# Kernel optimization log

Measured on AMD Instinct MI355X. Metric: run time of the kernel, lower is better.

## Reference

```python
import jax, jax.numpy as jnp
import numpy as np

N_CHUNK = 8
CHUNK = 128
HID = 1024

def cumsoftmax(x):
    return jnp.cumsum(jax.nn.softmax(x, axis=-1), axis=-1)

def setup_inputs() -> dict:
    key = jax.random.key(0)
    ks = jax.random.split(key, 4)
    L, B, D = 512, 64, HID
    G = 4 * HID + 2 * N_CHUNK  # 4112
    x = jax.random.normal(ks[0], (L, B, D), dtype=jnp.float32)
    h0 = jnp.zeros((2, B, HID), jnp.float32)
    c0 = jnp.zeros((2, B, N_CHUNK, CHUNK), jnp.float32)
    Wih = jax.random.normal(ks[1], (2, D, G), dtype=jnp.float32) * 0.02
    bih = jnp.zeros((2, G), jnp.float32)
    Whh = jax.random.normal(ks[2], (2, HID, G), dtype=jnp.float32) * 0.02
    bhh = jnp.zeros((2, G), jnp.float32)
    return {"x": x, "h0": h0, "c0": c0, "Wih": Wih, "bih": bih, "Whh": Whh, "bhh": bhh}

def _run_layer(prev, h, c, wih, b_ih, whh, b_hh):
    nc, cs = N_CHUNK, CHUNK
    # precompute input transform for all timesteps: [L,B,G]
    t_in = jnp.einsum('lbd,dg->lbg', prev, wih) + b_ih

    def step(carry, ti):
        hx, cx = carry
        gates = ti + hx @ whh + b_hh            # [B, G]
        cingate = 1.0 - cumsoftmax(gates[:, :nc])
        cforget = cumsoftmax(gates[:, nc:2 * nc])
        rest = gates[:, 2 * nc:].reshape(-1, 4 * nc, cs)
        outg, cell, ing, fg = jnp.split(rest, 4, axis=1)  # each [B,nc,cs]
        d_forget = 1.0 - cforget.sum(-1) / nc   # [B]? no: sum over nc -> [B]
        d_in = cingate.sum(-1) / nc
        cing = cingate[:, :, None]
        cfg = cforget[:, :, None]
        ing = jax.nn.sigmoid(ing)
        fg = jax.nn.sigmoid(fg)
        cell = jnp.tanh(cell)
        outg = jax.nn.sigmoid(outg)
        overlap = cfg * cing
        fg = fg * overlap + (cfg - overlap)
        ing = ing * overlap + (cing - overlap)
        cy = fg * cx + ing * cell
        hy = (outg * jnp.tanh(cy)).reshape(-1, HID)
        return (hy, cy), (hy, d_forget, d_in)

    (hT, cT), (hs, dfs, dins) = jax.lax.scan(step, (h, c), t_in)
    return hs, hT, cT, dfs, dins

def reference(x, h0, c0, Wih, bih, Whh, bhh):
    prev = x
    hTs, cTs, outs, dfs_l, dins_l = [], [], [], [], []
    for l in range(Wih.shape[0]):
        hs, hT, cT, dfs, dins = _run_layer(prev, h0[l], c0[l], Wih[l], bih[l], Whh[l], bhh[l])
        prev = hs  # dropout=0.0 / eval mode: LockedDropout is identity
        outs.append(hs)
        hTs.append(hT)
        cTs.append(cT)
        dfs_l.append(dfs)
        dins_l.append(dins)
    output = prev                                   # [L,B,H]
    return (output,
            jnp.stack(hTs), jnp.stack(cTs),         # final states per layer
            jnp.stack(outs),                        # raw_outputs == outputs (no dropout)
            jnp.stack(dfs_l), jnp.stack(dins_l))    # distances [n_layers,L,B]
```

## Files before the change

kernel.cpp:

```cpp
#include <hip/hip_runtime.h>
#include <math.h>

#define LSEQ 512
#define BATCH 64
#define HID 1024
#define NCH 8
#define GSZ 4112
#define NB2 128

typedef __bf16 bf16x8 __attribute__((ext_vector_type(8)));
typedef float f32x4 __attribute__((ext_vector_type(4)));
typedef unsigned u32x4 __attribute__((ext_vector_type(4)));
typedef unsigned u32x2 __attribute__((ext_vector_type(2)));

__device__ __forceinline__ ushort f2b(float f) {
  union { float f; unsigned u; } v; v.f = f;
  unsigned u = v.u;
  unsigned r = (u + 0x7FFFu + ((u >> 16) & 1u)) >> 16;
  return (ushort)r;
}
__device__ __forceinline__ float b2f(ushort h) {
  union { unsigned u; float f; } v; v.u = (unsigned)h << 16; return v.f;
}
__device__ __forceinline__ float sigmoidf(float x) { return 1.f / (1.f + expf(-x)); }

__global__ __launch_bounds__(256) void k_transpose_cast(
    const float* __restrict__ W, ushort* __restrict__ WT, int K, int N) {
  __shared__ float tile[32][33];
  int n0 = blockIdx.x * 32, k0 = blockIdx.y * 32;
  int tx = threadIdx.x & 31, ty = threadIdx.x >> 5;
  #pragma unroll
  for (int i = ty; i < 32; i += 8) {
    int n = n0 + tx;
    tile[i][tx] = (n < N) ? W[(size_t)(k0 + i) * N + n] : 0.f;
  }
  __syncthreads();
  #pragma unroll
  for (int i = ty; i < 32; i += 8) {
    int n = n0 + i;
    if (n < N) WT[(size_t)n * K + k0 + tx] = f2b(tile[tx][i]);
  }
}

__global__ void k_cast4(const float4* __restrict__ in, ushort* __restrict__ out, int count4) {
  int stride = gridDim.x * blockDim.x;
  for (int i = blockIdx.x * blockDim.x + threadIdx.x; i < count4; i += stride) {
    float4 v = in[i];
    ushort4 o;
    o.x = f2b(v.x); o.y = f2b(v.y); o.z = f2b(v.z); o.w = f2b(v.w);
    *reinterpret_cast<ushort4*>(out + (size_t)i * 4) = o;
  }
}

__global__ void k_init2(const float* __restrict__ h0, const float* __restrict__ c0,
                        ushort* __restrict__ h1b1, ushort* __restrict__ h2b1,
                        float* __restrict__ c1, float* __restrict__ c2,
                        unsigned* __restrict__ barmem) {
  int i = blockIdx.x * blockDim.x + threadIdx.x;
  const int n = BATCH * HID;
  if (i < n) { h1b1[i] = f2b(h0[i]); c1[i] = c0[i]; }
  else if (i < 2 * n) {
    int j = i - n;
    h2b1[j] = f2b(h0[n + j]); c2[j] = c0[n + j];
  }
  if (i < NB2 * 16) barmem[i] = 0u;
}

__global__ __launch_bounds__(256) void k_gemm_t(
    const ushort* __restrict__ A, const ushort* __restrict__ BT,
    const float* __restrict__ bias, ushort* __restrict__ Ct, int K, int N) {
  int col0 = blockIdx.x * 64;
  int t = blockIdx.y;
  int lane = threadIdx.x & 63;
  int w = threadIdx.x >> 6;
  int l15 = lane & 15;
  int koff = (lane >> 4) * 8;
  const ushort* Ap = A + (size_t)(t * 64 + w * 16 + l15) * K + koff;
  const ushort* Bp[4];
  int cols[4];
  #pragma unroll
  for (int cg = 0; cg < 4; ++cg) {
    int c_ = col0 + cg * 16 + l15;
    cols[cg] = c_;
    int cc = c_ < N ? c_ : N - 1;
    Bp[cg] = BT + (size_t)cc * K + koff;
  }
  f32x4 acc[4] = {};
  #pragma unroll 4
  for (int kk = 0; kk < K; kk += 32) {
    bf16x8 a = *reinterpret_cast<const bf16x8*>(Ap + kk);
    #pragma unroll
    for (int cg = 0; cg < 4; ++cg) {
      bf16x8 b = *reinterpret_cast<const bf16x8*>(Bp[cg] + kk);
      acc[cg] = __builtin_amdgcn_mfma_f32_16x16x32_bf16(a, b, acc[cg], 0, 0, 0);
    }
  }
  int crow = w * 16 + (lane >> 4) * 4;
  #pragma unroll
  for (int cg = 0; cg < 4; ++cg) {
    int c_ = cols[cg];
    if (c_ >= N) continue;
    float bv = bias[c_];
    ushort4 o;
    o.x = f2b(acc[cg][0] + bv); o.y = f2b(acc[cg][1] + bv);
    o.z = f2b(acc[cg][2] + bv); o.w = f2b(acc[cg][3] + bv);
    *reinterpret_cast<ushort4*>(&Ct[((size_t)t * GSZ + c_) * 64 + crow]) = o;
  }
}

__global__ __launch_bounds__(1024, 2) void k_scan2(
    const ushort* __restrict__ WhhT0, const ushort* __restrict__ WhhT1,
    const ushort* __restrict__ WihT1,
    const float* __restrict__ bhh0, const float* __restrict__ bhh1,
    const float* __restrict__ bih1,
    const ushort* __restrict__ tin,
    ushort* __restrict__ h1b0, ushort* __restrict__ h1b1,
    ushort* __restrict__ h2b0, ushort* __restrict__ h2b1,
    float* __restrict__ c1, float* __restrict__ c2,
    float* __restrict__ outs0, float* __restrict__ outs1,
    float* __restrict__ outdup,
    float* __restrict__ dfs0, float* __restrict__ dins0,
    float* __restrict__ dfs1, float* __restrict__ dins1,
    float* __restrict__ hT0, float* __restrict__ cT0,
    float* __restrict__ hT1, float* __restrict__ cT1,
    unsigned* __restrict__ barmem, int nsteps, int t0, int barbase) {
  __shared__ unsigned hlds[32768];
  __shared__ __align__(16) float gbuf[80][68];

  const int tid = threadIdx.x;
  const int blk = blockIdx.x;
  const bool isL2 = blk >= 64;
  const int lblk = isL2 ? (blk - 64) : blk;
  const int j0 = lblk * 16;
  const int lane = tid & 63;
  const int w = tid >> 6;
  const int l15 = lane & 15;
  const int lg = lane >> 4;
  const int koff = lg * 8;

  const int ct = (w < 5) ? w : 0;
  const int gcol = (ct == 0) ? l15 : (16 + (ct - 1) * 1024 + j0 + l15);
  const int grow = (ct == 0) ? l15 : (16 + (ct - 1) * 16 + l15);
  const ushort* bpA = (isL2 ? WhhT1 : WhhT0) + (size_t)gcol * HID + koff;
  const ushort* bpB = WihT1 + (size_t)gcol * HID + koff;
  const float bv = isL2 ? (bhh1[gcol] + bih1[gcol]) : bhh0[gcol];
  const int cr = lg * 4;
  const unsigned ab = (unsigned)l15 * 2048u + (unsigned)(lg * 16);
  const unsigned swz = (unsigned)(l15 & 7) << 4;

  const int cb = tid >> 4;
  const int jl = tid & 15;
  const int jglob = j0 + jl;
  const int rch = jglob >> 7;
  float creg = (isL2 ? c2 : c1)[cb * HID + jglob];

  float* out_my  = isL2 ? outs1 : outs0;
  float* dfs_my  = isL2 ? dfs1  : dfs0;
  float* dins_my = isL2 ? dins1 : dins0;

  float def_hy = 0.f, def_df = 0.f, def_di = 0.f;
  size_t def_oidx = 0;
  int def_didx = 0;
  bool have_def = false;

#define LOAD8(hbase) do { \
    const u32x4* hs_ = (const u32x4*)(hbase); \
    asm volatile("global_load_dwordx4 %0, %1, off sc0 sc1" : "=v"(z0) : "v"(hs_ + tid)        : "memory"); \
    asm volatile("global_load_dwordx4 %0, %1, off sc0 sc1" : "=v"(z1) : "v"(hs_ + tid + 1024) : "memory"); \
    asm volatile("global_load_dwordx4 %0, %1, off sc0 sc1" : "=v"(z2) : "v"(hs_ + tid + 2048) : "memory"); \
    asm volatile("global_load_dwordx4 %0, %1, off sc0 sc1" : "=v"(z3) : "v"(hs_ + tid + 3072) : "memory"); \
    asm volatile("global_load_dwordx4 %0, %1, off sc0 sc1" : "=v"(z4) : "v"(hs_ + tid + 4096) : "memory"); \
    asm volatile("global_load_dwordx4 %0, %1, off sc0 sc1" : "=v"(z5) : "v"(hs_ + tid + 5120) : "memory"); \
    asm volatile("global_load_dwordx4 %0, %1, off sc0 sc1" : "=v"(z6) : "v"(hs_ + tid + 6144) : "memory"); \
    asm volatile("global_load_dwordx4 %0, %1, off sc0 sc1" : "=v"(z7) : "v"(hs_ + tid + 7168) : "memory"); \
  } while (0)

#define WRITE8() do { \
    unsigned b_; \
    b_ = (unsigned)tid * 16u;          *(u32x4*)((char*)hlds + (b_ ^ (((b_ >> 11) & 7u) << 4))) = z0; \
    b_ = (unsigned)(tid + 1024) * 16u; *(u32x4*)((char*)hlds + (b_ ^ (((b_ >> 11) & 7u) << 4))) = z1; \
    b_ = (unsigned)(tid + 2048) * 16u; *(u32x4*)((char*)hlds + (b_ ^ (((b_ >> 11) & 7u) << 4))) = z2; \
    b_ = (unsigned)(tid + 3072) * 16u; *(u32x4*)((char*)hlds + (b_ ^ (((b_ >> 11) & 7u) << 4))) = z3; \
    b_ = (unsigned)(tid + 4096) * 16u; *(u32x4*)((char*)hlds + (b_ ^ (((b_ >> 11) & 7u) << 4))) = z4; \
    b_ = (unsigned)(tid + 5120) * 16u; *(u32x4*)((char*)hlds + (b_ ^ (((b_ >> 11) & 7u) << 4))) = z5; \
    b_ = (unsigned)(tid + 6144) * 16u; *(u32x4*)((char*)hlds + (b_ ^ (((b_ >> 11) & 7u) << 4))) = z6; \
    b_ = (unsigned)(tid + 7168) * 16u; *(u32x4*)((char*)hlds + (b_ ^ (((b_ >> 11) & 7u) << 4))) = z7; \
  } while (0)

#define GEMM_PASS(bp) do { \
    _Pragma("unroll 8") \
    for (int kb = 0; kb < 32; ++kb) { \
      bf16x8 b_ = *(const bf16x8*)((bp) + kb * 32); \
      unsigned o_ = ab + (unsigned)kb * 64u; \
      bf16x8 x0_ = *(const bf16x8*)((const char*)hlds + ((o_)           ^ swz)); \
      bf16x8 x1_ = *(const bf16x8*)((const char*)hlds + ((o_ + 32768u)  ^ swz)); \
      bf16x8 x2_ = *(const bf16x8*)((const char*)hlds + ((o_ + 65536u)  ^ swz)); \
      bf16x8 x3_ = *(const bf16x8*)((const char*)hlds + ((o_ + 98304u)  ^ swz)); \
      a0 = __builtin_amdgcn_mfma_f32_16x16x32_bf16(x0_, b_, a0, 0, 0, 0); \
      a1 = __builtin_amdgcn_mfma_f32_16x16x32_bf16(x1_, b_, a1, 0, 0, 0); \
      a2 = __builtin_amdgcn_mfma_f32_16x16x32_bf16(x2_, b_, a2, 0, 0, 0); \
      a3 = __builtin_amdgcn_mfma_f32_16x16x32_bf16(x3_, b_, a3, 0, 0, 0); \
    } \
  } while (0)

  for (int r = 0; r <= nsteps; ++r) {
    if (have_def) {
      asm volatile("global_store_dword %0, %1, off nt"
                   :: "v"(&out_my[def_oidx]), "v"(def_hy) : "memory");
      if (isL2)
        asm volatile("global_store_dword %0, %1, off nt"
                     :: "v"(&outdup[def_oidx]), "v"(def_hy) : "memory");
      if (lblk == 0 && jl == 0) {
        dfs_my[def_didx] = def_df;
        dins_my[def_didx] = def_di;
      }
      have_def = false;
    }

    const bool active = isL2 ? (r >= 1) : (r < nsteps);
    if (active) {
      const int t = isL2 ? (t0 + r - 1) : (t0 + r);
      const int tloc = isL2 ? (r - 1) : r;

      if (!isL2) {
        u32x4 z0, z1, z2, z3, z4, z5, z6, z7;
        LOAD8(((t - 1) & 1) ? h1b1 : h1b0);
        asm volatile("s_waitcnt vmcnt(0)" ::: "memory");
        __builtin_amdgcn_sched_barrier(0);
        WRITE8();
        __syncthreads();
        if (w < 5) {
          const ushort* tp = tin + ((size_t)tloc * GSZ + gcol) * 64 + cr;
          u32x2 q0, q1, q2, q3;
          asm volatile("global_load_dwordx2 %0, %1, off nt" : "=v"(q0) : "v"(tp)      : "memory");
          asm volatile("global_load_dwordx2 %0, %1, off nt" : "=v"(q1) : "v"(tp + 16) : "memory");
          asm volatile("global_load_dwordx2 %0, %1, off nt" : "=v"(q2) : "v"(tp + 32) : "memory");
          asm volatile("global_load_dwordx2 %0, %1, off nt" : "=v"(q3) : "v"(tp + 48) : "memory");
          f32x4 a0 = {}, a1 = {}, a2 = {}, a3 = {};
          GEMM_PASS(bpA);
          asm volatile("s_waitcnt vmcnt(0)" ::: "memory");
          __builtin_amdgcn_sched_barrier(0);
          ushort4 tv0, tv1, tv2, tv3;
          *(u32x2*)&tv0 = q0; *(u32x2*)&tv1 = q1;
          *(u32x2*)&tv2 = q2; *(u32x2*)&tv3 = q3;
          f32x4 g;
          g[0] = a0[0] + bv + b2f(tv0.x); g[1] = a0[1] + bv + b2f(tv0.y);
          g[2] = a0[2] + bv + b2f(tv0.z); g[3] = a0[3] + bv + b2f(tv0.w);
          *(f32x4*)(&gbuf[grow][cr]) = g;
          g[0] = a1[0] + bv + b2f(tv1.x); g[1] = a1[1] + bv + b2f(tv1.y);
          g[2] = a1[2] + bv + b2f(tv1.z); g[3] = a1[3] + bv + b2f(tv1.w);
          *(f32x4*)(&gbuf[grow][16 + cr]) = g;
          g[0] = a2[0] + bv + b2f(tv2.x); g[1] = a2[1] + bv + b2f(tv2.y);
          g[2] = a2[2] + bv + b2f(tv2.z); g[3] = a2[3] + bv + b2f(tv2.w);
          *(f32x4*)(&gbuf[grow][32 + cr]) = g;
          g[0] = a3[0] + bv + b2f(tv3.x); g[1] = a3[1] + bv + b2f(tv3.y);
          g[2] = a3[2] + bv + b2f(tv3.z); g[3] = a3[3] + bv + b2f(tv3.w);
          *(f32x4*)(&gbuf[grow][48 + cr]) = g;
        }
        __syncthreads();
      } else {
        f32x4 a0 = {}, a1 = {}, a2 = {}, a3 = {};
        {
          u32x4 z0, z1, z2, z3, z4, z5, z6, z7;
          LOAD8(((t - 1) & 1) ? h2b1 : h2b0);
          asm volatile("s_waitcnt vmcnt(0)" ::: "memory");
          __builtin_amdgcn_sched_barrier(0);
          WRITE8();
          __syncthreads();
        }
        {
          u32x4 z0, z1, z2, z3, z4, z5, z6, z7;
          LOAD8((t & 1) ? h1b1 : h1b0);
          if (w < 5) GEMM_PASS(bpA);
          asm volatile("s_waitcnt vmcnt(0)" ::: "memory");
          __builtin_amdgcn_sched_barrier(0);
          __syncthreads();
          WRITE8();
          __syncthreads();
        }
        if (w < 5) {
          GEMM_PASS(bpB);
          f32x4 g;
          g[0] = a0[0] + bv; g[1] = a0[1] + bv; g[2] = a0[2] + bv; g[3] = a0[3] + bv;
          *(f32x4*)(&gbuf[grow][cr]) = g;
          g[0] = a1[0] + bv; g[1] = a1[1] + bv; g[2] = a1[2] + bv; g[3] = a1[3] + bv;
          *(f32x4*)(&gbuf[grow][16 + cr]) = g;
          g[0] = a2[0] + bv; g[1] = a2[1] + bv; g[2] = a2[2] + bv; g[3] = a2[3] + bv;
          *(f32x4*)(&gbuf[grow][32 + cr]) = g;
          g[0] = a3[0] + bv; g[1] = a3[1] + bv; g[2] = a3[2] + bv; g[3] = a3[3] + bv;
          *(f32x4*)(&gbuf[grow][48 + cr]) = g;
        }
        __syncthreads();
      }

      float sm0[NCH], sm1[NCH];
      float m1 = -1e30f, m2 = -1e30f;
      #pragma unroll
      for (int i = 0; i < NCH; ++i) {
        sm0[i] = gbuf[i][cb];
        sm1[i] = gbuf[NCH + i][cb];
        m1 = fmaxf(m1, sm0[i]);
        m2 = fmaxf(m2, sm1[i]);
      }
      float s1 = 0.f, s2 = 0.f;
      #pragma unroll
      for (int i = 0; i < NCH; ++i) {
        sm0[i] = expf(sm0[i] - m1); s1 += sm0[i];
        sm1[i] = expf(sm1[i] - m2); s2 += sm1[i];
      }
      float r1 = 1.f / s1, r2 = 1.f / s2;
      float cum1 = 0.f, cum2 = 0.f, sumin = 0.f, sumfg = 0.f;
      float cing[NCH], cfg[NCH];
      #pragma unroll
      for (int i = 0; i < NCH; ++i) {
        cum1 += sm0[i] * r1; cing[i] = 1.f - cum1; sumin += cing[i];
        cum2 += sm1[i] * r2; cfg[i] = cum2; sumfg += cfg[i];
      }
      float go = gbuf[16 + jl][cb];
      float gc = gbuf[32 + jl][cb];
      float gi = gbuf[48 + jl][cb];
      float gf = gbuf[64 + jl][cb];
      float ov = cfg[rch] * cing[rch];
      float f_ = sigmoidf(gf) * ov + (cfg[rch] - ov);
      float i_ = sigmoidf(gi) * ov + (cing[rch] - ov);
      float cy = f_ * creg + i_ * tanhf(gc);
      float hy = sigmoidf(go) * tanhf(cy);
      creg = cy;

      ushort hv = f2b(hy);
      unsigned other = (unsigned)__shfl_xor((int)(unsigned)hv, 1, 64);
      ushort* ring = isL2 ? ((t & 1) ? h2b1 : h2b0) : ((t & 1) ? h1b1 : h1b0);
      ushort* hw = ring + cb * HID + jglob;
      if ((jl & 1) == 0) {
        unsigned pk = (unsigned)hv | (other << 16);
        asm volatile("global_store_dword %0, %1, off sc0 sc1" :: "v"(hw), "v"(pk) : "memory");
      }
      if (!isL2 && hT0 && r == nsteps - 1) {
        hT0[cb * HID + jglob] = hy; cT0[cb * HID + jglob] = cy;
      }
      if (isL2 && hT1 && r == nsteps) {
        hT1[cb * HID + jglob] = hy; cT1[cb * HID + jglob] = cy;
      }

      def_hy = hy;
      def_oidx = ((size_t)tloc * BATCH + cb) * HID + jglob;
      def_didx = tloc * BATCH + cb;
      def_df = 1.f - sumfg * 0.125f;
      def_di = sumin * 0.125f;
      have_def = true;
    }

    if (r < nsteps) {
      asm volatile("s_waitcnt vmcnt(0)" ::: "memory");
      __syncthreads();
      if (w == 0) {
        unsigned tgt = (unsigned)(barbase + r + 1);
        if (lane == 0) {
          unsigned* fp = barmem + (unsigned)blk * 16u;
          asm volatile("global_store_dword %0, %1, off sc0 sc1"
                       :: "v"(fp), "v"(tgt) : "memory");
        }
        const unsigned* mp0 = barmem + (unsigned)lane * 16u;
        const unsigned* mp1 = barmem + (unsigned)(64 + lane) * 16u;
        while (true) {
          unsigned f0, f1;
          asm volatile("global_load_dword %0, %1, off sc0 sc1"
                       : "=v"(f0) : "v"(mp0) : "memory");
          asm volatile("global_load_dword %0, %1, off sc0 sc1"
                       : "=v"(f1) : "v"(mp1) : "memory");
          asm volatile("s_waitcnt vmcnt(0)" ::: "memory");
          if (__all((int)(f0 >= tgt && f1 >= tgt))) break;
        }
      }
      __syncthreads();
    }
  }

  if (have_def) {
    out_my[def_oidx] = def_hy;
    if (isL2) outdup[def_oidx] = def_hy;
    if (lblk == 0 && jl == 0) {
      dfs_my[def_didx] = def_df;
      dins_my[def_didx] = def_di;
    }
  }
  (isL2 ? c2 : c1)[cb * HID + jglob] = creg;
#undef LOAD8
#undef WRITE8
#undef GEMM_PASS
}

extern "C" void kernel_launch(void* const* d_in, const int* in_sizes, int n_in,
                              void* d_out, int out_size, void* d_ws, size_t ws_size,
                              hipStream_t stream) {
  const float* x   = (const float*)d_in[0];
  const float* h0  = (const float*)d_in[1];
  const float* c0  = (const float*)d_in[2];
  const float* Wih = (const float*)d_in[3];
  const float* bih = (const float*)d_in[4];
  const float* Whh = (const float*)d_in[5];
  const float* bhh = (const float*)d_in[6];
  float* out = (float*)d_out;

  const size_t OFF_OUTPUT = 0;
  const size_t OFF_HT   = 33554432;
  const size_t OFF_CT   = OFF_HT + 131072;
  const size_t OFF_OUTS = OFF_CT + 131072;
  const size_t OFF_DFS  = OFF_OUTS + 67108864;
  const size_t OFF_DINS = OFF_DFS + 65536;

  uint8_t* ws = (uint8_t*)d_ws;
  size_t off = 0;
  auto alloc = [&](size_t bytes) { size_t p = off; off = (off + bytes + 255) & ~(size_t)255; return p; };
  const size_t wT_sz = (size_t)GSZ * HID * 2;
  size_t o_WihT[2], o_WhhT[2];
  o_WihT[0] = alloc(wT_sz); o_WihT[1] = alloc(wT_sz);
  o_WhhT[0] = alloc(wT_sz); o_WhhT[1] = alloc(wT_sz);
  size_t o_h1b0 = alloc((size_t)BATCH * HID * 2);
  size_t o_h1b1 = alloc((size_t)BATCH * HID * 2);
  size_t o_h2b0 = alloc((size_t)BATCH * HID * 2);
  size_t o_h2b1 = alloc((size_t)BATCH * HID * 2);
  size_t o_c1   = alloc((size_t)BATCH * HID * 4);
  size_t o_c2   = alloc((size_t)BATCH * HID * 4);
  size_t o_bar  = alloc(NB2 * 16 * 4);
  size_t fixed = off;
  const size_t unit = (size_t)BATCH * HID * 2 + (size_t)BATCH * GSZ * 2 + 512;
  int TC = 256;
  while (TC > 2 && fixed + (size_t)TC * unit > ws_size) TC >>= 1;
  size_t o_prevb = alloc((size_t)TC * BATCH * HID * 2);
  size_t o_tin   = alloc((size_t)TC * BATCH * GSZ * 2);

  ushort* h1b0 = (ushort*)(ws + o_h1b0);
  ushort* h1b1 = (ushort*)(ws + o_h1b1);
  ushort* h2b0 = (ushort*)(ws + o_h2b0);
  ushort* h2b1 = (ushort*)(ws + o_h2b1);
  float*  c1   = (float*)(ws + o_c1);
  float*  c2   = (float*)(ws + o_c2);
  unsigned* barmem = (unsigned*)(ws + o_bar);
  ushort* prevb = (ushort*)(ws + o_prevb);
  ushort* tin   = (ushort*)(ws + o_tin);

  dim3 tgrid((GSZ + 31) / 32, HID / 32);
  for (int l = 0; l < 2; ++l) {
    k_transpose_cast<<<tgrid, 256, 0, stream>>>(Wih + (size_t)l * HID * GSZ,
                                                (ushort*)(ws + o_WihT[l]), HID, GSZ);
    k_transpose_cast<<<tgrid, 256, 0, stream>>>(Whh + (size_t)l * HID * GSZ,
                                                (ushort*)(ws + o_WhhT[l]), HID, GSZ);
  }

  k_init2<<<(2 * BATCH * HID + 255) / 256, 256, 0, stream>>>(
      h0, c0, h1b1, h2b1, c1, c2, barmem);

  const int NB = (GSZ + 63) / 64;
  int barbase = 0;
  for (int t0 = 0; t0 < LSEQ; t0 += TC) {
    int nsteps = (LSEQ - t0 < TC) ? (LSEQ - t0) : TC;

    int count4 = nsteps * BATCH * HID / 4;
    int cblocks = (count4 + 255) / 256; if (cblocks > 2048) cblocks = 2048;
    k_cast4<<<cblocks, 256, 0, stream>>>(
        (const float4*)(x + (size_t)t0 * BATCH * HID), prevb, count4);
    k_gemm_t<<<dim3(NB, nsteps), 256, 0, stream>>>(prevb, (const ushort*)(ws + o_WihT[0]),
                                                   bih, tin, HID, GSZ);

    bool last = (t0 + nsteps == LSEQ);
    const ushort* WhhT0_p = (const ushort*)(ws + o_WhhT[0]);
    const ushort* WhhT1_p = (const ushort*)(ws + o_WhhT[1]);
    const ushort* WihT1_p = (const ushort*)(ws + o_WihT[1]);
    const float* bhh0_p = bhh;
    const float* bhh1_p = bhh + GSZ;
    const float* bih1_p = bih + GSZ;
    const ushort* tin_p = tin;
    float* outs0 = out + OFF_OUTS + (size_t)t0 * BATCH * HID;
    float* outs1 = out + OFF_OUTS + ((size_t)LSEQ + t0) * BATCH * HID;
    float* outdup = out + OFF_OUTPUT + (size_t)t0 * BATCH * HID;
    float* dfs0  = out + OFF_DFS  + (size_t)t0 * BATCH;
    float* dins0 = out + OFF_DINS + (size_t)t0 * BATCH;
    float* dfs1  = out + OFF_DFS  + ((size_t)LSEQ + t0) * BATCH;
    float* dins1 = out + OFF_DINS + ((size_t)LSEQ + t0) * BATCH;
    float* hT0 = last ? (out + OFF_HT) : nullptr;
    float* cT0 = last ? (out + OFF_CT) : nullptr;
    float* hT1 = last ? (out + OFF_HT + (size_t)BATCH * HID) : nullptr;
    float* cT1 = last ? (out + OFF_CT + (size_t)BATCH * HID) : nullptr;
    int nsteps_v = nsteps;
    int t0_v = t0;
    int barbase_v = barbase;

    void* args[] = {&WhhT0_p, &WhhT1_p, &WihT1_p, &bhh0_p, &bhh1_p, &bih1_p,
                    &tin_p, &h1b0, &h1b1, &h2b0, &h2b1, &c1, &c2,
                    &outs0, &outs1, &outdup, &dfs0, &dins0, &dfs1, &dins1,
                    &hT0, &cT0, &hT1, &cT1, &barmem, &nsteps_v, &t0_v, &barbase_v};
    hipLaunchCooperativeKernel((const void*)k_scan2, dim3(NB2), dim3(1024),
                               args, 0, stream);
    barbase += nsteps;
  }
}
```

Measured before the change: 12.06 ms.

## Use 32x32 MFMA in recurrent scan and LDS-tiled 128x128 input GEMM

After: 11.52 ms, median of 2. 4.4% less time.

```diff
diff --git a/kernel.cpp b/kernel.cpp
--- a/kernel.cpp
+++ b/kernel.cpp
@@ -10,6 +10,7 @@
 
 typedef __bf16 bf16x8 __attribute__((ext_vector_type(8)));
 typedef float f32x4 __attribute__((ext_vector_type(4)));
+typedef float f32x16 __attribute__((ext_vector_type(16)));
 typedef unsigned u32x4 __attribute__((ext_vector_type(4)));
 typedef unsigned u32x2 __attribute__((ext_vector_type(2)));
 
@@ -66,45 +67,80 @@
   if (i < NB2 * 16) barmem[i] = 0u;
 }
 
-__global__ __launch_bounds__(256) void k_gemm_t(
+__global__ __launch_bounds__(256, 3) void k_gemm_t2(
     const ushort* __restrict__ A, const ushort* __restrict__ BT,
-    const float* __restrict__ bias, ushort* __restrict__ Ct, int K, int N) {
-  int col0 = blockIdx.x * 64;
-  int t = blockIdx.y;
-  int lane = threadIdx.x & 63;
-  int w = threadIdx.x >> 6;
-  int l15 = lane & 15;
-  int koff = (lane >> 4) * 8;
-  const ushort* Ap = A + (size_t)(t * 64 + w * 16 + l15) * K + koff;
-  const ushort* Bp[4];
-  int cols[4];
+    const float* __restrict__ bias, ushort* __restrict__ Ct, int M) {
+  __shared__ ushort As[128 * 64];
+  __shared__ ushort Bs[128 * 64];
+  const int tid = threadIdx.x;
+  const int lane = tid & 63;
+  const int w = tid >> 6;
+  const int n0 = blockIdx.x * 128;
+  const int m0 = blockIdx.y * 128;
+  const int l15 = lane & 15;
+  const int lg = lane >> 4;
+  const int srow = tid >> 3;
+  const int scol = (tid & 7) * 8;
+  const int wr = w >> 1, wc = w & 1;
+
+  f32x4 acc[4][4] = {};
+
+  for (int kt = 0; kt < 1024; kt += 64) {
+    u32x4 av[4], bvv[4];
+    #pragma unroll
+    for (int i = 0; i < 4; ++i) {
+      int row = srow + i * 32;
+      av[i] = *(const u32x4*)(A + (size_t)(m0 + row) * 1024 + kt + scol);
+      int brow = n0 + row; if (brow >= GSZ) brow = GSZ - 1;
+      bvv[i] = *(const u32x4*)(BT + (size_t)brow * 1024 + kt + scol);
+    }
+    __syncthreads();
+    #pragma unroll
+    for (int i = 0; i < 4; ++i) {
+      int row = srow + i * 32;
+      unsigned L = (unsigned)row * 128u + (unsigned)scol * 2u;
+      unsigned Ls = L ^ ((unsigned)(row & 7) << 4);
+      *(u32x4*)((char*)As + Ls) = av[i];
+      *(u32x4*)((char*)Bs + Ls) = bvv[i];
+    }
+    __syncthreads();
+    #pragma unroll
+    for (int kk = 0; kk < 2; ++kk) {
+      bf16x8 af[4], bf[4];
+      #pragma unroll
+      for (int i = 0; i < 4; ++i) {
+        int arow = wr * 64 + i * 16 + l15;
+        unsigned L = (unsigned)arow * 128u + (unsigned)kk * 64u + (unsigned)lg * 16u;
+        af[i] = *(const bf16x8*)((const char*)As + (L ^ ((unsigned)(arow & 7) << 4)));
+        int bcol = wc * 64 + i * 16 + l15;
+        unsigned Lb = (unsigned)bcol * 128u + (unsigned)kk * 64u + (unsigned)lg * 16u;
+        bf[i] = *(const bf16x8*)((const char*)Bs + (Lb ^ ((unsigned)(bcol & 7) << 4)));
+      }
+      #pragma unroll
+      for (int i = 0; i < 4; ++i)
+        #pragma unroll
+        for (int j = 0; j < 4; ++j)
+          acc[i][j] = __builtin_amdgcn_mfma_f32_16x16x32_bf16(af[i], bf[j], acc[i][j], 0, 0, 0);
+    }
+  }
+
+  const int b4 = lg * 4;
   #pragma unroll
-  for (int cg = 0; cg < 4; ++cg) {
-    int c_ = col0 + cg * 16 + l15;
-    cols[cg] = c_;
-    int cc = c_ < N ? c_ : N - 1;
-    Bp[cg] = BT + (size_t)cc * K + koff;
-  }
-  f32x4 acc[4] = {};
-  #pragma unroll 4
-  for (int kk = 0; kk < K; kk += 32) {
-    bf16x8 a = *reinterpret_cast<const bf16x8*>(Ap + kk);
+  for (int i = 0; i < 4; ++i) {
+    int grow = m0 + wr * 64 + i * 16 + b4;
+    int t = grow >> 6;
+    int b = grow & 63;
     #pragma unroll
-    for (int cg = 0; cg < 4; ++cg) {
-      bf16x8 b = *reinterpret_cast<const bf16x8*>(Bp[cg] + kk);
-      acc[cg] = __builtin_amdgcn_mfma_f32_16x16x32_bf16(a, b, acc[cg], 0, 0, 0);
-    }
-  }
-  int crow = w * 16 + (lane >> 4) * 4;
-  #pragma unroll
-  for (int cg = 0; cg < 4; ++cg) {
-    int c_ = cols[cg];
-    if (c_ >= N) continue;
-    float bv = bias[c_];
-    ushort4 o;
-    o.x = f2b(acc[cg][0] + bv); o.y = f2b(acc[cg][1] + bv);
-    o.z = f2b(acc[cg][2] + bv); o.w = f2b(acc[cg][3] + bv);
-    *reinterpret_cast<ushort4*>(&Ct[((size_t)t * GSZ + c_) * 64 + crow]) = o;
+    for (int j = 0; j < 4; ++j) {
+      int col = n0 + wc * 64 + j * 16 + l15;
+      if (col < GSZ) {
+        float bb = bias[col];
+        ushort4 o;
+        o.x = f2b(acc[i][j][0] + bb); o.y = f2b(acc[i][j][1] + bb);
+        o.z = f2b(acc[i][j][2] + bb); o.w = f2b(acc[i][j][3] + bb);
+        *(ushort4*)(&Ct[((size_t)t * GSZ + col) * 64 + b]) = o;
+      }
+    }
   }
 }
 
@@ -125,7 +161,7 @@
     float* __restrict__ hT1, float* __restrict__ cT1,
     unsigned* __restrict__ barmem, int nsteps, int t0, int barbase) {
   __shared__ unsigned hlds[32768];
-  __shared__ __align__(16) float gbuf[80][68];
+  __shared__ __align__(16) float gbuf[96][68];
 
   const int tid = threadIdx.x;
   const int blk = blockIdx.x;
@@ -134,19 +170,20 @@
   const int j0 = lblk * 16;
   const int lane = tid & 63;
   const int w = tid >> 6;
-  const int l15 = lane & 15;
-  const int lg = lane >> 4;
-  const int koff = lg * 8;
-
-  const int ct = (w < 5) ? w : 0;
-  const int gcol = (ct == 0) ? l15 : (16 + (ct - 1) * 1024 + j0 + l15);
-  const int grow = (ct == 0) ? l15 : (16 + (ct - 1) * 16 + l15);
-  const ushort* bpA = (isL2 ? WhhT1 : WhhT0) + (size_t)gcol * HID + koff;
-  const ushort* bpB = WihT1 + (size_t)gcol * HID + koff;
-  const float bv = isL2 ? (bhh1[gcol] + bih1[gcol]) : bhh0[gcol];
-  const int cr = lg * 4;
-  const unsigned ab = (unsigned)l15 * 2048u + (unsigned)(lg * 16);
-  const unsigned swz = (unsigned)(l15 & 7) << 4;
+  const int l31 = lane & 31;
+  const int khalf = lane >> 5;
+
+  const int gc_ = (w < 3 ? w : 0) * 32 + l31;
+  int gcol32;
+  if (gc_ < 16)      gcol32 = gc_;
+  else if (gc_ < 80) gcol32 = 16 + ((gc_ - 16) >> 4) * 1024 + j0 + ((gc_ - 16) & 15);
+  else               gcol32 = 16 + 3 * 1024 + j0 + (gc_ - 80);
+  const ushort* bp32A = (isL2 ? WhhT1 : WhhT0) + (size_t)gcol32 * HID + khalf * 8;
+  const ushort* bp32B = WihT1 + (size_t)gcol32 * HID + khalf * 8;
+  const float bv32 = isL2 ? (bhh1[gcol32] + bih1[gcol32]) : bhh0[gcol32];
+  const unsigned a0base = (unsigned)l31 * 2048u + (unsigned)khalf * 16u;
+  const unsigned a1base = a0base + 32u * 2048u;
+  const unsigned swz32 = (unsigned)(l31 & 7) << 4;
 
   const int cb = tid >> 4;
   const int jl = tid & 15;
@@ -187,19 +224,27 @@
     b_ = (unsigned)(tid + 7168) * 16u; *(u32x4*)((char*)hlds + (b_ ^ (((b_ >> 11) & 7u) << 4))) = z7; \
   } while (0)
 
-#define GEMM_PASS(bp) do { \
+#define GEMM32(bp) do { \
     _Pragma("unroll 8") \
-    for (int kb = 0; kb < 32; ++kb) { \
-      bf16x8 b_ = *(const bf16x8*)((bp) + kb * 32); \
-      unsigned o_ = ab + (unsigned)kb * 64u; \
-      bf16x8 x0_ = *(const bf16x8*)((const char*)hlds + ((o_)           ^ swz)); \
-      bf16x8 x1_ = *(const bf16x8*)((const char*)hlds + ((o_ + 32768u)  ^ swz)); \
-      bf16x8 x2_ = *(const bf16x8*)((const char*)hlds + ((o_ + 65536u)  ^ swz)); \
-      bf16x8 x3_ = *(const bf16x8*)((const char*)hlds + ((o_ + 98304u)  ^ swz)); \
-      a0 = __builtin_amdgcn_mfma_f32_16x16x32_bf16(x0_, b_, a0, 0, 0, 0); \
-      a1 = __builtin_amdgcn_mfma_f32_16x16x32_bf16(x1_, b_, a1, 0, 0, 0); \
-      a2 = __builtin_amdgcn_mfma_f32_16x16x32_bf16(x2_, b_, a2, 0, 0, 0); \
-      a3 = __builtin_amdgcn_mfma_f32_16x16x32_bf16(x3_, b_, a3, 0, 0, 0); \
+    for (int ks = 0; ks < 64; ++ks) { \
+      bf16x8 b_ = *(const bf16x8*)((bp) + ks * 16); \
+      bf16x8 xA = *(const bf16x8*)((const char*)hlds + ((a0base + (unsigned)ks * 32u) ^ swz32)); \
+      bf16x8 xB = *(const bf16x8*)((const char*)hlds + ((a1base + (unsigned)ks * 32u) ^ swz32)); \
+      accA = __builtin_amdgcn_mfma_f32_32x32x16_bf16(xA, b_, accA, 0, 0, 0); \
+      accB = __builtin_amdgcn_mfma_f32_32x32x16_bf16(xB, b_, accB, 0, 0, 0); \
+    } \
+  } while (0)
+
+#define EPI_TILE(accX, bg, TQ) do { \
+    _Pragma("unroll") \
+    for (int q = 0; q < 4; ++q) { \
+      int rb = (bg) * 32 + q * 8 + khalf * 4; \
+      f32x4 g; \
+      g[0] = accX[q * 4 + 0] + bv32 TQ(q, 0); \
+      g[1] = accX[q * 4 + 1] + bv32 TQ(q, 1); \
+      g[2] = accX[q * 4 + 2] + bv32 TQ(q, 2); \
+      g[3] = accX[q * 4 + 3] + bv32 TQ(q, 3); \
+      *(f32x4*)(&gbuf[gc_][rb]) = g; \
     } \
   } while (0)
 
@@ -229,37 +274,30 @@
         __builtin_amdgcn_sched_barrier(0);
         WRITE8();
         __syncthreads();
-        if (w < 5) {
-          const ushort* tp = tin + ((size_t)tloc * GSZ + gcol) * 64 + cr;
-          u32x2 q0, q1, q2, q3;
-          asm volatile("global_load_dwordx2 %0, %1, off nt" : "=v"(q0) : "v"(tp)      : "memory");
-          asm volatile("global_load_dwordx2 %0, %1, off nt" : "=v"(q1) : "v"(tp + 16) : "memory");
-          asm volatile("global_load_dwordx2 %0, %1, off nt" : "=v"(q2) : "v"(tp + 32) : "memory");
-          asm volatile("global_load_dwordx2 %0, %1, off nt" : "=v"(q3) : "v"(tp + 48) : "memory");
-          f32x4 a0 = {}, a1 = {}, a2 = {}, a3 = {};
-          GEMM_PASS(bpA);
+        if (w < 3) {
+          const ushort* tp = tin + ((size_t)tloc * GSZ + gcol32) * 64 + khalf * 4;
+          u32x2 tq[8];
+          #pragma unroll
+          for (int q = 0; q < 8; ++q)
+            asm volatile("global_load_dwordx2 %0, %1, off nt"
+                         : "=v"(tq[q]) : "v"(tp + (q & 3) * 8 + (q >> 2) * 32) : "memory");
+          f32x16 accA = {}, accB = {};
+          GEMM32(bp32A);
           asm volatile("s_waitcnt vmcnt(0)" ::: "memory");
           __builtin_amdgcn_sched_barrier(0);
-          ushort4 tv0, tv1, tv2, tv3;
-          *(u32x2*)&tv0 = q0; *(u32x2*)&tv1 = q1;
-          *(u32x2*)&tv2 = q2; *(u32x2*)&tv3 = q3;
-          f32x4 g;
-          g[0] = a0[0] + bv + b2f(tv0.x); g[1] = a0[1] + bv + b2f(tv0.y);
-          g[2] = a0[2] + bv + b2f(tv0.z); g[3] = a0[3] + bv + b2f(tv0.w);
-          *(f32x4*)(&gbuf[grow][cr]) = g;
-          g[0] = a1[0] + bv + b2f(tv1.x); g[1] = a1[1] + bv + b2f(tv1.y);
-          g[2] = a1[2] + bv + b2f(tv1.z); g[3] = a1[3] + bv + b2f(tv1.w);
-          *(f32x4*)(&gbuf[grow][16 + cr]) = g;
-          g[0] = a2[0] + bv + b2f(tv2.x); g[1] = a2[1] + bv + b2f(tv2.y);
-          g[2] = a2[2] + bv + b2f(tv2.z); g[3] = a2[3] + bv + b2f(tv2.w);
-          *(f32x4*)(&gbuf[grow][32 + cr]) = g;
-          g[0] = a3[0] + bv + b2f(tv3.x); g[1] = a3[1] + bv + b2f(tv3.y);
-          g[2] = a3[2] + bv + b2f(tv3.z); g[3] = a3[3] + bv + b2f(tv3.w);
-          *(f32x4*)(&gbuf[grow][48 + cr]) = g;
+          ushort4 tu[8];
+          #pragma unroll
+          for (int q = 0; q < 8; ++q) *(u32x2*)&tu[q] = tq[q];
+#define TQA(q, ii) + b2f((&tu[q].x)[ii])
+#define TQB(q, ii) + b2f((&tu[4 + q].x)[ii])
+          EPI_TILE(accA, 0, TQA);
+          EPI_TILE(accB, 1, TQB);
+#undef TQA
+#undef TQB
         }
         __syncthreads();
       } else {
-        f32x4 a0 = {}, a1 = {}, a2 = {}, a3 = {};
+        f32x16 accA = {}, accB = {};
         {
           u32x4 z0, z1, z2, z3, z4, z5, z6, z7;
           LOAD8(((t - 1) & 1) ? h2b1 : h2b0);
@@ -271,24 +309,19 @@
         {
           u32x4 z0, z1, z2, z3, z4, z5, z6, z7;
           LOAD8((t & 1) ? h1b1 : h1b0);
-          if (w < 5) GEMM_PASS(bpA);
+          if (w < 3) GEMM32(bp32A);
           asm volatile("s_waitcnt vmcnt(0)" ::: "memory");
           __builtin_amdgcn_sched_barrier(0);
           __syncthreads();
           WRITE8();
           __syncthreads();
         }
-        if (w < 5) {
-          GEMM_PASS(bpB);
-          f32x4 g;
-          g[0] = a0[0] + bv; g[1] = a0[1] + bv; g[2] = a0[2] + bv; g[3] = a0[3] + bv;
-          *(f32x4*)(&gbuf[grow][cr]) = g;
-          g[0] = a1[0] + bv; g[1] = a1[1] + bv; g[2] = a1[2] + bv; g[3] = a1[3] + bv;
-          *(f32x4*)(&gbuf[grow][16 + cr]) = g;
-          g[0] = a2[0] + bv; g[1] = a2[1] + bv; g[2] = a2[2] + bv; g[3] = a2[3] + bv;
-          *(f32x4*)(&gbuf[grow][32 + cr]) = g;
-          g[0] = a3[0] + bv; g[1] = a3[1] + bv; g[2] = a3[2] + bv; g[3] = a3[3] + bv;
-          *(f32x4*)(&gbuf[grow][48 + cr]) = g;
+        if (w < 3) {
+          GEMM32(bp32B);
+#define TQN(q, ii)
+          EPI_TILE(accA, 0, TQN);
+          EPI_TILE(accB, 1, TQN);
+#undef TQN
         }
         __syncthreads();
       }
@@ -387,7 +420,8 @@
   (isL2 ? c2 : c1)[cb * HID + jglob] = creg;
 #undef LOAD8
 #undef WRITE8
-#undef GEMM_PASS
+#undef GEMM32
+#undef EPI_TILE
 }
 
 extern "C" void kernel_launch(void* const* d_in, const int* in_sizes, int n_in,
@@ -451,7 +485,6 @@
   k_init2<<<(2 * BATCH * HID + 255) / 256, 256, 0, stream>>>(
       h0, c0, h1b1, h2b1, c1, c2, barmem);
 
-  const int NB = (GSZ + 63) / 64;
   int barbase = 0;
   for (int t0 = 0; t0 < LSEQ; t0 += TC) {
     int nsteps = (LSEQ - t0 < TC) ? (LSEQ - t0) : TC;
@@ -460,8 +493,9 @@
     int cblocks = (count4 + 255) / 256; if (cblocks > 2048) cblocks = 2048;
     k_cast4<<<cblocks, 256, 0, stream>>>(
         (const float4*)(x + (size_t)t0 * BATCH * HID), prevb, count4);
-    k_gemm_t<<<dim3(NB, nsteps), 256, 0, stream>>>(prevb, (const ushort*)(ws + o_WihT[0]),
-                                                   bih, tin, HID, GSZ);
+    int M = nsteps * 64;
+    k_gemm_t2<<<dim3((GSZ + 127) / 128, M / 128), 256, 0, stream>>>(
+        prevb, (const ushort*)(ws + o_WihT[0]), bih, tin, M);
 
     bool last = (t0 + nsteps == LSEQ);
     const ushort* WhhT0_p = (const ushort*)(ws + o_WhhT[0]);
```
